# Kernel tuning notes

Measured on AMD Instinct MI355X. Metric: run time of the kernel, lower is better.

## Reference

```python
import jax, jax.numpy as jnp
import numpy as np

B, L, E, H = 2, 2048, 1024, 16
D = E // H
EPS = 1e-5


def setup_inputs() -> dict:
    key = jax.random.key(0)
    ks = jax.random.split(key, 12)
    s = 1.0 / np.sqrt(E)
    x = jax.random.normal(ks[0], (B, L, E), dtype=jnp.float32)
    # bool mask: True = block. Causal upper-triangular mask (L, S) with S == L.
    mask = jnp.triu(jnp.ones((L, L), dtype=jnp.bool_), k=1)
    Wq = jax.random.normal(ks[1], (E, E), jnp.float32) * s
    bq = jax.random.normal(ks[2], (E,), jnp.float32) * 0.01
    Wk = jax.random.normal(ks[3], (E, E), jnp.float32) * s
    bk = jax.random.normal(ks[4], (E,), jnp.float32) * 0.01
    Wv = jax.random.normal(ks[5], (E, E), jnp.float32) * s
    bv = jax.random.normal(ks[6], (E,), jnp.float32) * 0.01
    Wo = jax.random.normal(ks[7], (E, E), jnp.float32) * s
    bo = jax.random.normal(ks[8], (E,), jnp.float32) * 0.01
    gamma = jnp.ones((E,), jnp.float32)
    beta = jnp.zeros((E,), jnp.float32)
    return {"x": x, "mask": mask, "Wq": Wq, "bq": bq, "Wk": Wk, "bk": bk,
            "Wv": Wv, "bv": bv, "Wo": Wo, "bo": bo, "gamma": gamma, "beta": beta}


def reference(x, mask, Wq, bq, Wk, bk, Wv, bv, Wo, bo, gamma, beta):
    b, l, e = x.shape
    x = jnp.nan_to_num(x, nan=0.0, posinf=1e9, neginf=-1e9)
    # QKV projections (torch Linear: x @ W.T + b), split heads -> (B,H,L,D)
    q = (x @ Wq.T + bq).reshape(b, l, H, D).transpose(0, 2, 1, 3)
    k = (x @ Wk.T + bk).reshape(b, l, H, D).transpose(0, 2, 1, 3)
    v = (x @ Wv.T + bv).reshape(b, l, H, D).transpose(0, 2, 1, 3)
    scale = max(D ** 0.5, 1e-6)
    scores = jnp.einsum('bhtd,bhsd->bhts', q, k) / scale  # (B,H,L,L)
    # bool mask True=block -> additive -inf, broadcast (L,L) over (B,H)
    scores = scores + jnp.where(mask, -jnp.inf, 0.0).astype(scores.dtype)
    scores = scores - jnp.max(scores, axis=-1, keepdims=True)
    scores = jnp.nan_to_num(scores, nan=0.0, posinf=1e9, neginf=-1e9)
    attn = jax.nn.softmax(scores, axis=-1)
    o = jnp.einsum('bhts,bhsd->bhtd', attn, v)
    o = o.transpose(0, 2, 1, 3).reshape(b, l, e)
    y = o @ Wo.T + bo
    r = y + x
    # LayerNorm over last dim
    mu = jnp.mean(r, axis=-1, keepdims=True)
    var = jnp.mean((r - mu) ** 2, axis=-1, keepdims=True)
    out = (r - mu) * jax.lax.rsqrt(var + EPS) * gamma + beta
    out = jnp.nan_to_num(out, nan=0.0, posinf=1e9, neginf=-1e9)
    return out
```

## Files before the change

### kernel.cpp

```cpp
#include <hip/hip_runtime.h>
#include <hip/hip_bf16.h>
#include <cstdint>
#include <cstddef>

#define NB 2
#define NL 2048
#define NE 1024
#define NH 16
#define ND 64
#define NM (NB * NL)

typedef float f32x4 __attribute__((ext_vector_type(4)));
typedef __bf16 bf16x8 __attribute__((ext_vector_type(8)));
typedef __bf16 bf16x4 __attribute__((ext_vector_type(4)));

#define DEV static __device__ __forceinline__

DEV f32x4 mfma16(bf16x8 a, bf16x8 b, f32x4 c) {
  return __builtin_amdgcn_mfma_f32_16x16x32_bf16(a, b, c, 0, 0, 0);
}

DEV ushort f2bf(float f) {
  uint32_t u = __float_as_uint(f);
  uint32_t r = (u + 0x7fffu + ((u >> 16) & 1u)) >> 16;
  return (ushort)r;
}

DEV float bf2f(ushort u) { return __uint_as_float((uint32_t)u << 16); }

#if __has_builtin(__builtin_amdgcn_exp2f)
DEV float fast_exp2(float x) { return __builtin_amdgcn_exp2f(x); }
#else
DEV float fast_exp2(float x) { return exp2f(x); }
#endif

DEV void gl_lds16(const void* src, void* lds_dst) {
  __builtin_amdgcn_global_load_lds(
      (const __attribute__((address_space(1))) void*)src,
      (__attribute__((address_space(3))) void*)lds_dst, 16, 0, 0);
}

template <int NCALLS>
DEV void stage_swz(const char* gbase, size_t row_stride_b, char* lds_base, int tid) {
#pragma unroll
  for (int c = 0; c < NCALLS; ++c) {
    uint32_t P = (uint32_t)(c * 4096 + tid * 16);
    uint32_t r = P >> 7;
    uint32_t Lo = P ^ ((r & 7u) << 4);
    gl_lds16(gbase + (size_t)r * row_stride_b + (Lo & 127u), lds_base + P);
  }
}

__global__ __launch_bounds__(256) void pack_kernel(
    const float* __restrict__ x, const float* __restrict__ wq,
    const float* __restrict__ wk, const float* __restrict__ wv,
    const float* __restrict__ wo, ushort* __restrict__ xb,
    ushort* __restrict__ wqb, ushort* __restrict__ wkb,
    ushort* __restrict__ wvb, ushort* __restrict__ wob) {
  int64_t q = (int64_t)blockIdx.x * 256 + threadIdx.x;
  const float* src;
  ushort* dst;
  bool cl;
  if (q < 1048576) {
    src = x + q * 4;
    dst = xb + q * 4;
    cl = true;
  } else {
    int64_t r = q - 1048576;
    int wsel = (int)(r >> 18);
    int64_t o = (r & 262143) * 4;
    cl = false;
    if (wsel == 0) { src = wq + o; dst = wqb + o; }
    else if (wsel == 1) { src = wk + o; dst = wkb + o; }
    else if (wsel == 2) { src = wv + o; dst = wvb + o; }
    else { src = wo + o; dst = wob + o; }
  }
  float4 v = *(const float4*)src;
  if (cl) {
    v.x = (v.x != v.x) ? 0.f : fminf(fmaxf(v.x, -1e9f), 1e9f);
    v.y = (v.y != v.y) ? 0.f : fminf(fmaxf(v.y, -1e9f), 1e9f);
    v.z = (v.z != v.z) ? 0.f : fminf(fmaxf(v.z, -1e9f), 1e9f);
    v.w = (v.w != v.w) ? 0.f : fminf(fmaxf(v.w, -1e9f), 1e9f);
  }
  ushort4 o4;
  o4.x = f2bf(v.x);
  o4.y = f2bf(v.y);
  o4.z = f2bf(v.z);
  o4.w = f2bf(v.w);
  *(ushort4*)dst = o4;
}

__global__ __launch_bounds__(256) void qkv_gemm_kernel(
    const ushort* __restrict__ xb, const ushort* __restrict__ wqb,
    const ushort* __restrict__ wkb, const ushort* __restrict__ wvb,
    const float* __restrict__ bq, const float* __restrict__ bk,
    const float* __restrict__ bv, ushort* __restrict__ Qo,
    ushort* __restrict__ Ko, ushort* __restrict__ Vto) {
  __shared__ __align__(128) char lds[65536];
  const int tid = threadIdx.x;
  const int w = tid >> 6, ln = tid & 63;
  const int ln15 = ln & 15, g = ln >> 4;
  const int wm = w >> 1, wn = w & 1;
  const int m0 = blockIdx.y * 128;
  const int which = blockIdx.x >> 3;
  const int n0w = (blockIdx.x & 7) * 128;
  const ushort* Wb = (which == 0) ? wqb : (which == 1) ? wkb : wvb;

  const char* Abase = (const char*)xb + (size_t)m0 * 2048;
  const char* Bbase = (const char*)Wb + (size_t)n0w * 2048;

  f32x4 acc[4][4];
#pragma unroll
  for (int m = 0; m < 4; ++m)
#pragma unroll
    for (int n = 0; n < 4; ++n) acc[m][n] = {0.f, 0.f, 0.f, 0.f};

  int cur = 0;
  stage_swz<4>(Abase, 2048, lds, tid);
  stage_swz<4>(Bbase, 2048, lds + 32768, tid);

  for (int kt = 0; kt < 16; ++kt) {
    if (kt + 1 < 16) {
      stage_swz<4>(Abase + (kt + 1) * 128, 2048, lds + (cur ^ 1) * 16384, tid);
      stage_swz<4>(Bbase + (kt + 1) * 128, 2048,
                   lds + 32768 + (cur ^ 1) * 16384, tid);
      asm volatile("s_waitcnt vmcnt(8)" ::: "memory");
    } else {
      asm volatile("s_waitcnt vmcnt(0)" ::: "memory");
    }
    __builtin_amdgcn_s_barrier();
    asm volatile("" ::: "memory");
    const char* ab = lds + cur * 16384;
    const char* bb = lds + 32768 + cur * 16384;
    __builtin_amdgcn_s_setprio(1);
#pragma unroll
    for (int kc = 0; kc < 2; ++kc) {
      bf16x8 af[4], bfr[4];
#pragma unroll
      for (int i = 0; i < 4; ++i) {
        uint32_t ar = (uint32_t)(wm * 64 + i * 16 + ln15);
        uint32_t ao = (ar * 128u + (uint32_t)(kc * 64 + g * 16)) ^ ((ar & 7u) << 4);
        af[i] = *(const bf16x8*)(ab + ao);
        uint32_t br = (uint32_t)(wn * 64 + i * 16 + ln15);
        uint32_t bo_ = (br * 128u + (uint32_t)(kc * 64 + g * 16)) ^ ((br & 7u) << 4);
        bfr[i] = *(const bf16x8*)(bb + bo_);
      }
#pragma unroll
      for (int m = 0; m < 4; ++m)
#pragma unroll
        for (int n = 0; n < 4; ++n) acc[m][n] = mfma16(af[m], bfr[n], acc[m][n]);
    }
    __builtin_amdgcn_s_setprio(0);
    asm volatile("s_waitcnt lgkmcnt(0)" ::: "memory");
    __builtin_amdgcn_s_barrier();
    asm volatile("" ::: "memory");
    cur ^= 1;
  }

  const float* bias = (which == 0) ? bq : (which == 1) ? bk : bv;
  const float sc = (which == 0) ? 0.18033688011112042f : 1.0f;
#pragma unroll
  for (int n = 0; n < 4; ++n) {
    const int col = n0w + wn * 64 + n * 16 + ln15;
    const int h = col >> 6, d = col & 63;
    const float bc = bias[col];
#pragma unroll
    for (int m = 0; m < 4; ++m) {
      if (which < 2) {
        ushort* dst = (which == 0) ? Qo : Ko;
#pragma unroll
        for (int j = 0; j < 4; ++j) {
          int mg = m0 + wm * 64 + m * 16 + g * 4 + j;
          int b = mg >> 11, l = mg & 2047;
          dst[((size_t)(b * NH + h) * NL + l) * ND + d] = f2bf((acc[m][n][j] + bc) * sc);
        }
      } else {
        int mg0 = m0 + wm * 64 + m * 16 + g * 4;
        int b = mg0 >> 11, l0 = mg0 & 2047;
        ushort4 pk;
        pk.x = f2bf(acc[m][n][0] + bc);
        pk.y = f2bf(acc[m][n][1] + bc);
        pk.z = f2bf(acc[m][n][2] + bc);
        pk.w = f2bf(acc[m][n][3] + bc);
        *(ushort4*)(Vto + ((size_t)(b * NH + h) * ND + d) * NL + l0) = pk;
      }
    }
  }
}

__global__ __launch_bounds__(256) void attn_kernel(
    const ushort* __restrict__ Q, const ushort* __restrict__ K,
    const ushort* __restrict__ Vt, ushort* __restrict__ Op,
    ushort* __restrict__ po, float* __restrict__ pml) {
  __shared__ __align__(128) char lds[40960];
  const int tid = threadIdx.x;
  const int w = tid >> 6, ln = tid & 63;
  const int ln15 = ln & 15, g = ln >> 4;
  const int bx = blockIdx.x;
  const int bh = bx & 31;
  const int seg = bx >> 5;
  int qt, ci;
  if (seg < 17) {
    qt = 31 - seg;
    ci = 0;
  } else if (seg == 17) {
    qt = 31; ci = 1;
  } else {
    const int k = seg - 18;
    const int L = 15 - (k >> 1);
    if ((k & 1) == 0) { qt = L + 15; ci = 1; }
    else             { qt = L - 1;  ci = 0; }
  }
  const int nt = qt + 1;
  const int lo = ci * 16;
  const int hi = (nt < lo + 16) ? nt : lo + 16;

  const int b = bh >> 4, h = bh & 15;
  const ushort* Qh = Q + (size_t)bh * NL * ND;
  const ushort* Kh = K + (size_t)bh * NL * ND;
  const ushort* Vth = Vt + (size_t)bh * ND * NL;
  const uint32_t pbase = 32768u + (uint32_t)w * 2048u;

  const int q0 = qt * 64;
  const int r0 = q0 + w * 16;

  bf16x8 qf[2];
#pragma unroll
  for (int kc = 0; kc < 2; ++kc)
    qf[kc] = *(const bf16x8*)(Qh + (size_t)(r0 + ln15) * ND + kc * 32 + g * 8);

  f32x4 o_acc[4];
#pragma unroll
  for (int n = 0; n < 4; ++n) o_acc[n] = {0.f, 0.f, 0.f, 0.f};
  float m_run = -1e30f, l_run = 0.f;

  int cur = 0;
  stage_swz<2>((const char*)Kh + (size_t)lo * 64 * 128, 128, lds, tid);
  stage_swz<2>((const char*)Vth + (size_t)lo * 64 * 2, (size_t)NL * 2, lds + 16384, tid);

  for (int t = lo; t < hi; ++t) {
    const int s0 = t * 64;
    asm volatile("s_waitcnt vmcnt(0)" ::: "memory");
    __builtin_amdgcn_s_barrier();
    asm volatile("" ::: "memory");
    if (t + 1 < hi) {
      stage_swz<2>((const char*)Kh + (size_t)(s0 + 64) * 128, 128,
                   lds + (cur ^ 1) * 8192, tid);
      stage_swz<2>((const char*)Vth + (size_t)(s0 + 64) * 2, (size_t)NL * 2,
                   lds + 16384 + (cur ^ 1) * 8192, tid);
    }

    const char* kb = lds + cur * 8192;
    const char* vb = lds + 16384 + cur * 8192;

    f32x4 s_acc[4];
#pragma unroll
    for (int n = 0; n < 4; ++n) s_acc[n] = {0.f, 0.f, 0.f, 0.f};
    __builtin_amdgcn_s_setprio(1);
#pragma unroll
    for (int kc = 0; kc < 2; ++kc) {
      bf16x8 kf[4];
#pragma unroll
      for (int n = 0; n < 4; ++n) {
        uint32_t kr = (uint32_t)(n * 16 + ln15);
        uint32_t off = (kr * 128u + (uint32_t)(kc * 64 + g * 16)) ^ ((kr & 7u) << 4);
        kf[n] = *(const bf16x8*)(kb + off);
      }
#pragma unroll
      for (int n = 0; n < 4; ++n) s_acc[n] = mfma16(kf[n], qf[kc], s_acc[n]);
    }
    __builtin_amdgcn_s_setprio(0);

    if (t == nt - 1) {
      const int qi = r0 + ln15;
#pragma unroll
      for (int n = 0; n < 4; ++n)
#pragma unroll
        for (int j = 0; j < 4; ++j) {
          int si = s0 + n * 16 + g * 4 + j;
          s_acc[n][j] = (si > qi) ? -1e30f : s_acc[n][j];
        }
    }

    float mx;
    {
      float a0 = fmaxf(fmaxf(s_acc[0][0], s_acc[0][1]), s_acc[0][2]);
      float a1 = fmaxf(fmaxf(s_acc[0][3], s_acc[1][0]), s_acc[1][1]);
      float a2 = fmaxf(fmaxf(s_acc[1][2], s_acc[1][3]), s_acc[2][0]);
      float a3 = fmaxf(fmaxf(s_acc[2][1], s_acc[2][2]), s_acc[2][3]);
      float a4 = fmaxf(fmaxf(s_acc[3][0], s_acc[3][1]), s_acc[3][2]);
      float b0 = fmaxf(fmaxf(a0, a1), a2);
      float b1 = fmaxf(fmaxf(a3, a4), s_acc[3][3]);
      mx = fmaxf(b0, b1);
    }
    if (__any(mx > m_run + 8.0f)) {
      float mr = fmaxf(mx, __shfl_xor(mx, 16));
      mr = fmaxf(mr, __shfl_xor(mr, 32));
      float mn = fmaxf(m_run, mr);
      float al = fast_exp2(m_run - mn);
      m_run = mn;
      l_run *= al;
#pragma unroll
      for (int j = 0; j < 4; ++j) {
        float aj = __shfl(al, g * 4 + j);
#pragma unroll
        for (int n = 0; n < 4; ++n) o_acc[n][j] *= aj;
      }
    }
    float ps = 0.f;
#pragma unroll
    for (int n = 0; n < 4; ++n) {
      float p0 = fast_exp2(s_acc[n][0] - m_run);
      float p1 = fast_exp2(s_acc[n][1] - m_run);
      float p2 = fast_exp2(s_acc[n][2] - m_run);
      float p3 = fast_exp2(s_acc[n][3] - m_run);
      ps += (p0 + p1) + (p2 + p3);
      bf16x4 pk = {(__bf16)p0, (__bf16)p1, (__bf16)p2, (__bf16)p3};
      uint32_t off = ((uint32_t)ln15 * 128u + (uint32_t)(n * 32 + g * 8)) ^
                     (((uint32_t)ln15 & 7u) << 4);
      *(bf16x4*)(lds + pbase + off) = pk;
    }
    l_run += ps;

    __builtin_amdgcn_s_setprio(1);
#pragma unroll
    for (int kc = 0; kc < 2; ++kc) {
      uint32_t poff = ((uint32_t)ln15 * 128u + (uint32_t)(kc * 64 + g * 16)) ^
                      (((uint32_t)ln15 & 7u) << 4);
      bf16x8 pf = *(const bf16x8*)(lds + pbase + poff);
      bf16x8 vf[4];
#pragma unroll
      for (int n = 0; n < 4; ++n) {
        uint32_t vr = (uint32_t)(n * 16 + ln15);
        uint32_t off = (vr * 128u + (uint32_t)(kc * 64 + g * 16)) ^ ((vr & 7u) << 4);
        vf[n] = *(const bf16x8*)(vb + off);
      }
#pragma unroll
      for (int n = 0; n < 4; ++n) o_acc[n] = mfma16(pf, vf[n], o_acc[n]);
    }
    __builtin_amdgcn_s_setprio(0);
    cur ^= 1;
  }

  l_run += __shfl_xor(l_run, 16);
  l_run += __shfl_xor(l_run, 32);

  if (nt <= 16) {
    float invl = 1.0f / l_run;
#pragma unroll
    for (int j = 0; j < 4; ++j) {
      float inv = __shfl(invl, g * 4 + j);
      int qi = r0 + g * 4 + j;
      size_t rowo = ((size_t)b * NL + qi) * NE + h * ND;
#pragma unroll
      for (int n = 0; n < 4; ++n) Op[rowo + n * 16 + ln15] = f2bf(o_acc[n][j] * inv);
    }
  } else {
    const int slot = (bh * 16 + (qt - 16)) * 2 + ci;
    ushort* so = po + (size_t)slot * 4096;
#pragma unroll
    for (int j = 0; j < 4; ++j) {
      int ql = w * 16 + g * 4 + j;
#pragma unroll
      for (int n = 0; n < 4; ++n) so[ql * 64 + n * 16 + ln15] = f2bf(o_acc[n][j]);
    }
    if (g == 0) {
      pml[(size_t)slot * 128 + (w * 16 + ln15) * 2] = m_run;
      pml[(size_t)slot * 128 + (w * 16 + ln15) * 2 + 1] = l_run;
    }
  }
}

__global__ __launch_bounds__(256) void attn_combine_kernel(
    const ushort* __restrict__ po, const float* __restrict__ pml,
    ushort* __restrict__ Op) {
  const int bx = blockIdx.x;
  const int qt = 16 + (bx >> 5), bh = bx & 31;
  const int b = bh >> 4, h = bh & 15;
  const int tid = threadIdx.x;
  const int row = tid >> 2, dseg = (tid & 3) * 16;
  const int slot = (bh * 16 + (qt - 16)) * 2;
  const float* ml1 = pml + (size_t)slot * 128 + row * 2;
  const float* ml2 = pml + (size_t)(slot + 1) * 128 + row * 2;
  const float m1 = ml1[0], l1 = ml1[1];
  const float m2 = ml2[0], l2 = ml2[1];
  const float M = fmaxf(m1, m2);
  const float w1 = fast_exp2(m1 - M), w2 = fast_exp2(m2 - M);
  const float inv = 1.0f / (w1 * l1 + w2 * l2);
  const ushort* o1 = po + (size_t)slot * 4096 + row * 64 + dseg;
  const ushort* o2 = po + (size_t)(slot + 1) * 4096 + row * 64 + dseg;
  ushort4 r1a = *(const ushort4*)o1, r1b = *(const ushort4*)(o1 + 4);
  ushort4 r1c = *(const ushort4*)(o1 + 8), r1d = *(const ushort4*)(o1 + 12);
  ushort4 r2a = *(const ushort4*)o2, r2b = *(const ushort4*)(o2 + 4);
  ushort4 r2c = *(const ushort4*)(o2 + 8), r2d = *(const ushort4*)(o2 + 12);
  ushort out[16];
  ushort q1[16] = {r1a.x, r1a.y, r1a.z, r1a.w, r1b.x, r1b.y, r1b.z, r1b.w,
                   r1c.x, r1c.y, r1c.z, r1c.w, r1d.x, r1d.y, r1d.z, r1d.w};
  ushort q2[16] = {r2a.x, r2a.y, r2a.z, r2a.w, r2b.x, r2b.y, r2b.z, r2b.w,
                   r2c.x, r2c.y, r2c.z, r2c.w, r2d.x, r2d.y, r2d.z, r2d.w};
#pragma unroll
  for (int i = 0; i < 16; ++i)
    out[i] = f2bf((w1 * bf2f(q1[i]) + w2 * bf2f(q2[i])) * inv);
  ushort* dst = Op + ((size_t)(b * NL + qt * 64 + row)) * NE + h * ND + dseg;
#pragma unroll
  for (int i = 0; i < 4; ++i)
    *(ushort4*)(dst + i * 4) = *(ushort4*)(out + i * 4);
}

__global__ __launch_bounds__(256) void oproj_kernel(
    const ushort* __restrict__ ob, const ushort* __restrict__ wob,
    const float* __restrict__ bo, const float* __restrict__ x,
    float* __restrict__ out) {
  __shared__ __align__(128) char lds[65536];
  const int tid = threadIdx.x;
  const int w = tid >> 6, ln = tid & 63;
  const int ln15 = ln & 15, g = ln >> 4;
  const int wm = w >> 1, wn = w & 1;
  const int m0 = blockIdx.y * 128;
  const int n0 = blockIdx.x * 128;

  const char* Abase = (const char*)ob + (size_t)m0 * 2048;
  const char* Bbase = (const char*)wob + (size_t)n0 * 2048;

  f32x4 acc[4][4];
#pragma unroll
  for (int m = 0; m < 4; ++m)
#pragma unroll
    for (int n = 0; n < 4; ++n) acc[m][n] = {0.f, 0.f, 0.f, 0.f};

  int cur = 0;
  stage_swz<4>(Abase, 2048, lds, tid);
  stage_swz<4>(Bbase, 2048, lds + 32768, tid);

  for (int kt = 0; kt < 16; ++kt) {
    if (kt + 1 < 16) {
      stage_swz<4>(Abase + (kt + 1) * 128, 2048, lds + (cur ^ 1) * 16384, tid);
      stage_swz<4>(Bbase + (kt + 1) * 128, 2048,
                   lds + 32768 + (cur ^ 1) * 16384, tid);
      asm volatile("s_waitcnt vmcnt(8)" ::: "memory");
    } else {
      asm volatile("s_waitcnt vmcnt(0)" ::: "memory");
    }
    __builtin_amdgcn_s_barrier();
    asm volatile("" ::: "memory");
    const char* ab = lds + cur * 16384;
    const char* bb = lds + 32768 + cur * 16384;
    __builtin_amdgcn_s_setprio(1);
#pragma unroll
    for (int kc = 0; kc < 2; ++kc) {
      bf16x8 af[4], bfr[4];
#pragma unroll
      for (int i = 0; i < 4; ++i) {
        uint32_t ar = (uint32_t)(wm * 64 + i * 16 + ln15);
        uint32_t ao = (ar * 128u + (uint32_t)(kc * 64 + g * 16)) ^ ((ar & 7u) << 4);
        af[i] = *(const bf16x8*)(ab + ao);
        uint32_t br = (uint32_t)(wn * 64 + i * 16 + ln15);
        uint32_t bo_ = (br * 128u + (uint32_t)(kc * 64 + g * 16)) ^ ((br & 7u) << 4);
        bfr[i] = *(const bf16x8*)(bb + bo_);
      }
#pragma unroll
      for (int m = 0; m < 4; ++m)
#pragma unroll
        for (int n = 0; n < 4; ++n) acc[m][n] = mfma16(af[m], bfr[n], acc[m][n]);
    }
    __builtin_amdgcn_s_setprio(0);
    asm volatile("s_waitcnt lgkmcnt(0)" ::: "memory");
    __builtin_amdgcn_s_barrier();
    asm volatile("" ::: "memory");
    cur ^= 1;
  }

#pragma unroll
  for (int n = 0; n < 4; ++n) {
    const int col = n0 + wn * 64 + n * 16 + ln15;
    const float bc = bo[col];
#pragma unroll
    for (int m = 0; m < 4; ++m)
#pragma unroll
      for (int j = 0; j < 4; ++j) {
        int mg = m0 + wm * 64 + m * 16 + g * 4 + j;
        size_t idx = (size_t)mg * NE + col;
        out[idx] = acc[m][n][j] + bc + x[idx];
      }
  }
}

__global__ __launch_bounds__(256) void ln_kernel(float* __restrict__ io,
                                                 const float* __restrict__ gamma,
                                                 const float* __restrict__ beta) {
  const int row = blockIdx.x, tid = threadIdx.x;
  const int w = tid >> 6, ln = tid & 63;
  float4 v = *(const float4*)(io + (size_t)row * NE + tid * 4);
  float s = v.x + v.y + v.z + v.w;
  float ss = v.x * v.x + v.y * v.y + v.z * v.z + v.w * v.w;
#pragma unroll
  for (int d = 1; d < 64; d <<= 1) {
    s += __shfl_xor(s, d);
    ss += __shfl_xor(ss, d);
  }
  __shared__ float red[8];
  if (ln == 0) {
    red[w] = s;
    red[4 + w] = ss;
  }
  __syncthreads();
  s = red[0] + red[1] + red[2] + red[3];
  ss = red[4] + red[5] + red[6] + red[7];
  const float mu = s * (1.0f / (float)NE);
  float var = ss * (1.0f / (float)NE) - mu * mu;
  const float inv = rsqrtf(var + 1e-5f);
  float4 gv = *(const float4*)(gamma + tid * 4);
  float4 bv = *(const float4*)(beta + tid * 4);
  float4 o;
  o.x = (v.x - mu) * inv * gv.x + bv.x;
  o.y = (v.y - mu) * inv * gv.y + bv.y;
  o.z = (v.z - mu) * inv * gv.z + bv.z;
  o.w = (v.w - mu) * inv * gv.w + bv.w;
  *(float4*)(io + (size_t)row * NE + tid * 4) = o;
}

extern "C" void kernel_launch(void* const* d_in, const int* in_sizes, int n_in,
                              void* d_out, int out_size, void* d_ws, size_t ws_size,
                              hipStream_t stream) {
  const float* x = (const float*)d_in[0];
  const float* Wq = (const float*)d_in[2];
  const float* bq = (const float*)d_in[3];
  const float* Wk = (const float*)d_in[4];
  const float* bk = (const float*)d_in[5];
  const float* Wv = (const float*)d_in[6];
  const float* bv = (const float*)d_in[7];
  const float* Wo = (const float*)d_in[8];
  const float* bo = (const float*)d_in[9];
  const float* gamma = (const float*)d_in[10];
  const float* beta = (const float*)d_in[11];

  char* ws = (char*)d_ws;
  ushort* xb  = (ushort*)(ws + 0);
  ushort* wqb = (ushort*)(ws + 8388608);
  ushort* wkb = (ushort*)(ws + 10485760);
  ushort* wvb = (ushort*)(ws + 12582912);
  ushort* wob = (ushort*)(ws + 14680064);
  ushort* Qb  = (ushort*)(ws + 16777216);
  ushort* Kb  = (ushort*)(ws + 25165824);
  ushort* Vtb = (ushort*)(ws + 33554432);
  ushort* Ob  = (ushort*)(ws + 41943040);
  ushort* po  = (ushort*)(ws + 0);
  float*  pml = (float*)(ws + 8388608);

  pack_kernel<<<8192, 256, 0, stream>>>(x, Wq, Wk, Wv, Wo, xb, wqb, wkb, wvb, wob);
  qkv_gemm_kernel<<<dim3(24, 32), 256, 0, stream>>>(xb, wqb, wkb, wvb, bq, bk, bv,
                                                    Qb, Kb, Vtb);
  attn_kernel<<<1536, 256, 0, stream>>>(Qb, Kb, Vtb, Ob, po, pml);
  attn_combine_kernel<<<512, 256, 0, stream>>>(po, pml, Ob);
  oproj_kernel<<<dim3(8, 32), 256, 0, stream>>>(Ob, wob, bo, x, (float*)d_out);
  ln_kernel<<<4096, 256, 0, stream>>>((float*)d_out, gamma, beta);
}
```

Baseline: 110.2 us.

## Load GEMM B operand directly to registers and halve LDS for occupancy

In the QKV and output-projection GEMMs, the weight (B) tiles are now read from global memory straight into registers with a double-buffered register prefetch. Only the activation (A) tile still goes through swizzled LDS, which halves the LDS footprint, and launch bounds request three blocks per CU. The aim is to cut LDS traffic and raise occupancy. The cost is extra register pressure, a full vmcnt(0) wait at each stage, and less coalesced per-lane global loads of B that are duplicated across the wm wave pair.

```diff
diff --git a/kernel.cpp b/kernel.cpp
--- a/kernel.cpp
+++ b/kernel.cpp
@@ -90,13 +90,39 @@
   *(ushort4*)dst = o4;
 }
 
-__global__ __launch_bounds__(256) void qkv_gemm_kernel(
+#define GEMM_LOADB(R, t_)                                                     \
+  do {                                                                        \
+    _Pragma("unroll") for (int kc = 0; kc < 2; ++kc)                          \
+        _Pragma("unroll") for (int i = 0; i < 4; ++i)                         \
+            R[kc][i] = *(const bf16x8*)(Bq + (size_t)(i * 16) * 1024 +        \
+                                        (t_) * 64 + kc * 32);                 \
+  } while (0)
+
+#define GEMM_COMP(BUF, R)                                                     \
+  do {                                                                        \
+    __builtin_amdgcn_s_setprio(1);                                            \
+    _Pragma("unroll") for (int kc = 0; kc < 2; ++kc) {                        \
+      bf16x8 af[4];                                                           \
+      _Pragma("unroll") for (int i = 0; i < 4; ++i) {                         \
+        uint32_t ar = (uint32_t)(wm * 64 + i * 16 + ln15);                    \
+        uint32_t ao = (ar * 128u + (uint32_t)(kc * 64 + g * 16)) ^            \
+                      ((ar & 7u) << 4);                                       \
+        af[i] = *(const bf16x8*)((BUF) + ao);                                 \
+      }                                                                       \
+      _Pragma("unroll") for (int m = 0; m < 4; ++m)                           \
+          _Pragma("unroll") for (int n = 0; n < 4; ++n)                       \
+              acc[m][n] = mfma16(af[m], R[kc][n], acc[m][n]);                 \
+    }                                                                         \
+    __builtin_amdgcn_s_setprio(0);                                            \
+  } while (0)
+
+__global__ __launch_bounds__(256, 3) void qkv_gemm_kernel(
     const ushort* __restrict__ xb, const ushort* __restrict__ wqb,
     const ushort* __restrict__ wkb, const ushort* __restrict__ wvb,
     const float* __restrict__ bq, const float* __restrict__ bk,
     const float* __restrict__ bv, ushort* __restrict__ Qo,
     ushort* __restrict__ Ko, ushort* __restrict__ Vto) {
-  __shared__ __align__(128) char lds[65536];
+  __shared__ __align__(128) char lds[32768];
   const int tid = threadIdx.x;
   const int w = tid >> 6, ln = tid & 63;
   const int ln15 = ln & 15, g = ln >> 4;
@@ -107,7 +133,7 @@
   const ushort* Wb = (which == 0) ? wqb : (which == 1) ? wkb : wvb;
 
   const char* Abase = (const char*)xb + (size_t)m0 * 2048;
-  const char* Bbase = (const char*)Wb + (size_t)n0w * 2048;
+  const ushort* Bq = Wb + (size_t)(n0w + wn * 64 + ln15) * 1024 + g * 8;
 
   f32x4 acc[4][4];
 #pragma unroll
@@ -115,46 +141,25 @@
 #pragma unroll
     for (int n = 0; n < 4; ++n) acc[m][n] = {0.f, 0.f, 0.f, 0.f};
 
-  int cur = 0;
+  bf16x8 brA[2][4], brB[2][4];
   stage_swz<4>(Abase, 2048, lds, tid);
-  stage_swz<4>(Bbase, 2048, lds + 32768, tid);
-
-  for (int kt = 0; kt < 16; ++kt) {
-    if (kt + 1 < 16) {
-      stage_swz<4>(Abase + (kt + 1) * 128, 2048, lds + (cur ^ 1) * 16384, tid);
-      stage_swz<4>(Bbase + (kt + 1) * 128, 2048,
-                   lds + 32768 + (cur ^ 1) * 16384, tid);
-      asm volatile("s_waitcnt vmcnt(8)" ::: "memory");
-    } else {
-      asm volatile("s_waitcnt vmcnt(0)" ::: "memory");
-    }
+  GEMM_LOADB(brA, 0);
+
+  for (int kt = 0; kt < 16; kt += 2) {
+    asm volatile("s_waitcnt vmcnt(0)" ::: "memory");
     __builtin_amdgcn_s_barrier();
     asm volatile("" ::: "memory");
-    const char* ab = lds + cur * 16384;
-    const char* bb = lds + 32768 + cur * 16384;
-    __builtin_amdgcn_s_setprio(1);
-#pragma unroll
-    for (int kc = 0; kc < 2; ++kc) {
-      bf16x8 af[4], bfr[4];
-#pragma unroll
-      for (int i = 0; i < 4; ++i) {
-        uint32_t ar = (uint32_t)(wm * 64 + i * 16 + ln15);
-        uint32_t ao = (ar * 128u + (uint32_t)(kc * 64 + g * 16)) ^ ((ar & 7u) << 4);
-        af[i] = *(const bf16x8*)(ab + ao);
-        uint32_t br = (uint32_t)(wn * 64 + i * 16 + ln15);
-        uint32_t bo_ = (br * 128u + (uint32_t)(kc * 64 + g * 16)) ^ ((br & 7u) << 4);
-        bfr[i] = *(const bf16x8*)(bb + bo_);
-      }
-#pragma unroll
-      for (int m = 0; m < 4; ++m)
-#pragma unroll
-        for (int n = 0; n < 4; ++n) acc[m][n] = mfma16(af[m], bfr[n], acc[m][n]);
-    }
-    __builtin_amdgcn_s_setprio(0);
-    asm volatile("s_waitcnt lgkmcnt(0)" ::: "memory");
+    stage_swz<4>(Abase + (kt + 1) * 128, 2048, lds + 16384, tid);
+    GEMM_LOADB(brB, kt + 1);
+    GEMM_COMP(lds, brA);
+    asm volatile("s_waitcnt vmcnt(0)" ::: "memory");
     __builtin_amdgcn_s_barrier();
     asm volatile("" ::: "memory");
-    cur ^= 1;
+    if (kt + 2 < 16) {
+      stage_swz<4>(Abase + (kt + 2) * 128, 2048, lds, tid);
+      GEMM_LOADB(brA, kt + 2);
+    }
+    GEMM_COMP(lds + 16384, brB);
   }
 
   const float* bias = (which == 0) ? bq : (which == 1) ? bk : bv;
@@ -407,11 +412,11 @@
     *(ushort4*)(dst + i * 4) = *(ushort4*)(out + i * 4);
 }
 
-__global__ __launch_bounds__(256) void oproj_kernel(
+__global__ __launch_bounds__(256, 3) void oproj_kernel(
     const ushort* __restrict__ ob, const ushort* __restrict__ wob,
     const float* __restrict__ bo, const float* __restrict__ x,
     float* __restrict__ out) {
-  __shared__ __align__(128) char lds[65536];
+  __shared__ __align__(128) char lds[32768];
   const int tid = threadIdx.x;
   const int w = tid >> 6, ln = tid & 63;
   const int ln15 = ln & 15, g = ln >> 4;
@@ -420,7 +425,7 @@
   const int n0 = blockIdx.x * 128;
 
   const char* Abase = (const char*)ob + (size_t)m0 * 2048;
-  const char* Bbase = (const char*)wob + (size_t)n0 * 2048;
+  const ushort* Bq = wob + (size_t)(n0 + wn * 64 + ln15) * 1024 + g * 8;
 
   f32x4 acc[4][4];
 #pragma unroll
@@ -428,46 +433,25 @@
 #pragma unroll
     for (int n = 0; n < 4; ++n) acc[m][n] = {0.f, 0.f, 0.f, 0.f};
 
-  int cur = 0;
+  bf16x8 brA[2][4], brB[2][4];
   stage_swz<4>(Abase, 2048, lds, tid);
-  stage_swz<4>(Bbase, 2048, lds + 32768, tid);
-
-  for (int kt = 0; kt < 16; ++kt) {
-    if (kt + 1 < 16) {
-      stage_swz<4>(Abase + (kt + 1) * 128, 2048, lds + (cur ^ 1) * 16384, tid);
-      stage_swz<4>(Bbase + (kt + 1) * 128, 2048,
-                   lds + 32768 + (cur ^ 1) * 16384, tid);
-      asm volatile("s_waitcnt vmcnt(8)" ::: "memory");
-    } else {
-      asm volatile("s_waitcnt vmcnt(0)" ::: "memory");
-    }
+  GEMM_LOADB(brA, 0);
+
+  for (int kt = 0; kt < 16; kt += 2) {
+    asm volatile("s_waitcnt vmcnt(0)" ::: "memory");
     __builtin_amdgcn_s_barrier();
     asm volatile("" ::: "memory");
-    const char* ab = lds + cur * 16384;
-    const char* bb = lds + 32768 + cur * 16384;
-    __builtin_amdgcn_s_setprio(1);
-#pragma unroll
-    for (int kc = 0; kc < 2; ++kc) {
-      bf16x8 af[4], bfr[4];
-#pragma unroll
-      for (int i = 0; i < 4; ++i) {
-        uint32_t ar = (uint32_t)(wm * 64 + i * 16 + ln15);
-        uint32_t ao = (ar * 128u + (uint32_t)(kc * 64 + g * 16)) ^ ((ar & 7u) << 4);
-        af[i] = *(const bf16x8*)(ab + ao);
-        uint32_t br = (uint32_t)(wn * 64 + i * 16 + ln15);
-        uint32_t bo_ = (br * 128u + (uint32_t)(kc * 64 + g * 16)) ^ ((br & 7u) << 4);
-        bfr[i] = *(const bf16x8*)(bb + bo_);
-      }
-#pragma unroll
-      for (int m = 0; m < 4; ++m)
-#pragma unroll
-        for (int n = 0; n < 4; ++n) acc[m][n] = mfma16(af[m], bfr[n], acc[m][n]);
-    }
-    __builtin_amdgcn_s_setprio(0);
-    asm volatile("s_waitcnt lgkmcnt(0)" ::: "memory");
+    stage_swz<4>(Abase + (kt + 1) * 128, 2048, lds + 16384, tid);
+    GEMM_LOADB(brB, kt + 1);
+    GEMM_COMP(lds, brA);
+    asm volatile("s_waitcnt vmcnt(0)" ::: "memory");
     __builtin_amdgcn_s_barrier();
     asm volatile("" ::: "memory");
-    cur ^= 1;
+    if (kt + 2 < 16) {
+      stage_swz<4>(Abase + (kt + 2) * 128, 2048, lds, tid);
+      GEMM_LOADB(brA, kt + 2);
+    }
+    GEMM_COMP(lds + 16384, brB);
   }
 
 #pragma unroll
```

Result: slower. 184.4 us (+67.3%).
